# Performance work log

Hardware: AMD Instinct MI355X
Metric: run time of the kernel (lower is better)

Reference implementation:

```python
import jax, jax.numpy as jnp
import numpy as np

ALPHA = 0.2  # LeakyReLU negative slope
NEG_FILL = -9e15


def setup_inputs() -> dict:
    key = jax.random.key(0)
    k_adj, k_x, k_W, k_a = jax.random.split(key, 4)
    n, in_feats, out_feats = 12288, 256, 64
    adj = jax.random.randint(k_adj, (n, n), 0, 2, dtype=jnp.int32)
    x = jax.random.normal(k_x, (n, in_feats), dtype=jnp.float32)
    W = jax.random.normal(k_W, (in_feats, out_feats), dtype=jnp.float32) * 0.1
    a = jax.random.normal(k_a, (2 * out_feats, 1), dtype=jnp.float32) * 0.1
    return {"adj": adj, "x": x, "W": W, "a": a}


def reference(adj, x, W, a):
    out_feats = W.shape[1]
    h = x @ W                                  # (n, out_feats)
    wh1 = h @ a[:out_feats]                    # (n, 1)
    wh2 = h @ a[out_feats:]                    # (n, 1)
    e = jax.nn.leaky_relu(wh1 + wh2, ALPHA)    # (n, 1) -- faithful to source (no transpose)
    # broadcast (n,1) scores against (n,n) adjacency mask
    attention = jnp.where(adj > 0, e, NEG_FILL)
    attention = jax.nn.softmax(attention, axis=1)
    # dropout p=0.0 -> identity (eval mode)
    h_prime = attention @ h                    # (n, out_feats)
    return jax.nn.elu(h_prime)                 # concat=True
```

## Files before the change

### kernel.cpp

```cpp
#include <hip/hip_runtime.h>

#define N_NODES 12288
#define IN_F    256
#define OUT_F   64
#define KSPLIT  32
#define MT      64
#define KC      (N_NODES / KSPLIT)
#define NSTRH   (N_NODES + 32)
#define ABSTR   1600

typedef __attribute__((ext_vector_type(8))) short bf16x8;
typedef __attribute__((ext_vector_type(4))) float f32x4;

__device__ __forceinline__ unsigned short f2bf(float f) {
    union { float f; unsigned int i; } v; v.f = f;
    unsigned int x = v.i;
    unsigned int r = x + 0x7FFFu + ((x >> 16) & 1u);
    return (unsigned short)(r >> 16);
}

__global__ __launch_bounds__(256) void k_bitpack(const int* __restrict__ adj,
                                                 unsigned char* __restrict__ abits) {
    const int tid  = threadIdx.x;
    const int lane = tid & 63;
    const int wave = tid >> 6;
    const int row  = blockIdx.x * 2 + (wave >> 1);
    const int half = wave & 1;

    const int* src = adj + (size_t)row * N_NODES + half * (N_NODES / 2) + lane;
    unsigned long long* dst =
        (unsigned long long*)(abits + (size_t)row * ABSTR + half * (N_NODES / 16));

    const int iters = (N_NODES / 2) / 64;
    int a0 = src[0];
    int a1 = src[64];
    for (int i = 0; i < iters - 2; ++i) {
        int a2 = src[(size_t)(i + 2) * 64];
        unsigned long long m = __ballot(a0 != 0);
        if (lane == 0) dst[i] = m;
        a0 = a1; a1 = a2;
    }
    unsigned long long m0 = __ballot(a0 != 0);
    unsigned long long m1 = __ballot(a1 != 0);
    if (lane == 0) { dst[iters - 2] = m0; dst[iters - 1] = m1; }
}

__global__ __launch_bounds__(256) void k_hT(const float* __restrict__ x,
                                            const float* __restrict__ W,
                                            unsigned short* __restrict__ hT) {
    __shared__ unsigned short WT[OUT_F][IN_F + 8];
    int tid = threadIdx.x;
    for (int idx = tid; idx < IN_F * OUT_F; idx += 256) {
        int k = idx >> 6, n = idx & 63;
        WT[n][k] = f2bf(W[idx]);
    }
    __syncthreads();

    int lane = tid & 63, wave = tid >> 6;
    int q = lane >> 4, ml = lane & 15;
    int i0 = blockIdx.x * MT;
    int row = i0 + 16 * wave + ml;
    const float* xr = x + (size_t)row * IN_F + 8 * q;

    f32x4 acc[4];
    #pragma unroll
    for (int nt = 0; nt < 4; ++nt) acc[nt] = (f32x4){0.f, 0.f, 0.f, 0.f};

    #pragma unroll
    for (int kk = 0; kk < IN_F; kk += 32) {
        float4 x0 = *(const float4*)(xr + kk);
        float4 x1 = *(const float4*)(xr + kk + 4);
        union { bf16x8 v; unsigned short u[8]; } A;
        A.u[0] = f2bf(x0.x); A.u[1] = f2bf(x0.y); A.u[2] = f2bf(x0.z); A.u[3] = f2bf(x0.w);
        A.u[4] = f2bf(x1.x); A.u[5] = f2bf(x1.y); A.u[6] = f2bf(x1.z); A.u[7] = f2bf(x1.w);
        #pragma unroll
        for (int nt = 0; nt < 4; ++nt) {
            bf16x8 bv = *(const bf16x8*)&WT[16 * nt + ml][kk + 8 * q];
            acc[nt] = __builtin_amdgcn_mfma_f32_16x16x32_bf16(A.v, bv, acc[nt], 0, 0, 0);
        }
    }

    #pragma unroll
    for (int nt = 0; nt < 4; ++nt) {
        ushort4 o;
        o.x = f2bf(acc[nt][0]); o.y = f2bf(acc[nt][1]);
        o.z = f2bf(acc[nt][2]); o.w = f2bf(acc[nt][3]);
        *(ushort4*)&hT[(size_t)(16 * nt + ml) * NSTRH + i0 + 16 * wave + 4 * q] = o;
    }
}

__global__ __launch_bounds__(256) void k_spmm(const unsigned char* __restrict__ abits,
                                              const unsigned short* __restrict__ hT,
                                              float* __restrict__ s_part,
                                              float* __restrict__ deg_part) {
    __shared__ unsigned short Bs[OUT_F][KC + 8];
    __shared__ unsigned char  Ab[MT][52];

    const int tid  = threadIdx.x;
    const int lane = tid & 63;
    const int wave = tid >> 6;
    const int q    = lane >> 4;
    const int ml   = lane & 15;
    const int i0   = blockIdx.x * MT;
    const int ks   = blockIdx.y;
    const int k0   = ks * KC;

    {
        const int brow = 16 * wave + (lane >> 2);
        const int bco  = (lane & 3) * 8;
        const unsigned short* bp = hT + (size_t)brow * NSTRH + k0 + bco;
        #pragma unroll
        for (int j = 0; j < 12; ++j) {
            uint4 v = *(const uint4*)(bp + 32 * j);
            *(uint4*)&Bs[brow][bco + 32 * j] = v;
        }
    }
    {
        const int arow = tid >> 2;
        const int apart = (tid & 3) * 12;
        const unsigned int* asrc =
            (const unsigned int*)(abits + (size_t)(i0 + arow) * ABSTR + ks * (KC / 8) + apart);
        unsigned int d0 = asrc[0], d1 = asrc[1], d2 = asrc[2];
        unsigned int* ad = (unsigned int*)&Ab[arow][apart];
        ad[0] = d0; ad[1] = d1; ad[2] = d2;
    }
    __syncthreads();

    union { bf16x8 v; unsigned short u[8]; } ones;
    #pragma unroll
    for (int i = 0; i < 8; ++i) ones.u[i] = 0x3F80;

    f32x4 acc[4], accd;
    #pragma unroll
    for (int nt = 0; nt < 4; ++nt) acc[nt] = (f32x4){0.f, 0.f, 0.f, 0.f};
    accd = (f32x4){0.f, 0.f, 0.f, 0.f};

    const int arow = 16 * wave + ml;
    #pragma unroll
    for (int kk = 0; kk < KC; kk += 32) {
        unsigned int b = Ab[arow][(kk >> 3) + q];
        union { bf16x8 v; unsigned int w[4]; } av;
        av.w[0] = (b & 1u) * 0x3F80u         + (b & 2u) * 0x1FC00000u;
        av.w[1] = ((b >> 2) & 1u) * 0x3F80u  + ((b >> 2) & 2u) * 0x1FC00000u;
        av.w[2] = ((b >> 4) & 1u) * 0x3F80u  + ((b >> 4) & 2u) * 0x1FC00000u;
        av.w[3] = ((b >> 6) & 1u) * 0x3F80u  + ((b >> 6) & 2u) * 0x1FC00000u;

        #pragma unroll
        for (int nt = 0; nt < 4; ++nt) {
            bf16x8 bv = *(const bf16x8*)&Bs[16 * nt + ml][kk + 8 * q];
            acc[nt] = __builtin_amdgcn_mfma_f32_16x16x32_bf16(av.v, bv, acc[nt], 0, 0, 0);
        }
        accd = __builtin_amdgcn_mfma_f32_16x16x32_bf16(av.v, ones.v, accd, 0, 0, 0);
    }

    float* sp = s_part + (size_t)ks * ((size_t)N_NODES * OUT_F);
    #pragma unroll
    for (int nt = 0; nt < 4; ++nt) {
        #pragma unroll
        for (int rr = 0; rr < 4; ++rr) {
            int orow = i0 + 16 * wave + 4 * q + rr;
            int ocol = 16 * nt + ml;
            sp[(size_t)orow * OUT_F + ocol] = acc[nt][rr];
        }
    }

    if (ml == 0) {
        #pragma unroll
        for (int rr = 0; rr < 4; ++rr)
            deg_part[ks * N_NODES + i0 + 16 * wave + 4 * q + rr] = accd[rr];
    }
}

__global__ __launch_bounds__(256) void k_out(const float* __restrict__ s_part,
                                             const float* __restrict__ deg_part,
                                             float* __restrict__ out) {
    int idx = blockIdx.x * 256 + threadIdx.x;
    int i = idx >> 6;
    float s = 0.f, deg = 0.f;
    #pragma unroll
    for (int p = 0; p < KSPLIT; ++p) {
        s   += s_part[(size_t)p * ((size_t)N_NODES * OUT_F) + idx];
        deg += deg_part[p * N_NODES + i];
    }
    float v = (deg > 0.5f) ? (s / deg) : 0.f;
    out[idx] = (v > 0.f) ? v : expm1f(v);
}

extern "C" void kernel_launch(void* const* d_in, const int* in_sizes, int n_in,
                              void* d_out, int out_size, void* d_ws, size_t ws_size,
                              hipStream_t stream) {
    const int*   adj = (const int*)d_in[0];
    const float* x   = (const float*)d_in[1];
    const float* W   = (const float*)d_in[2];
    float* out = (float*)d_out;

    char* ws = (char*)d_ws;
    const size_t hT_bytes = (size_t)OUT_F * NSTRH * 2;
    const size_t sp_bytes = (size_t)KSPLIT * N_NODES * OUT_F * 4;
    const size_t dp_bytes = (size_t)KSPLIT * N_NODES * 4;
    unsigned short* hT   = (unsigned short*)ws;
    float* s_part        = (float*)(ws + hT_bytes);
    float* deg_part      = (float*)(ws + hT_bytes + sp_bytes);
    unsigned char* abits = (unsigned char*)(ws + hT_bytes + sp_bytes + dp_bytes);

    k_bitpack<<<dim3(N_NODES / 2),          dim3(256), 0, stream>>>(adj, abits);
    k_hT     <<<dim3(N_NODES / MT),         dim3(256), 0, stream>>>(x, W, hT);
    k_spmm   <<<dim3(N_NODES / MT, KSPLIT), dim3(256), 0, stream>>>(abits, hT, s_part, deg_part);
    k_out    <<<dim3(N_NODES * OUT_F / 256),dim3(256), 0, stream>>>(s_part, deg_part, out);
}
```

Before: 878.9 us.

## Restructure adjacency bitpack as persistent grid-stride kernel with dense bit layout

The bit-packing kernel now runs as a fixed grid of 2048 blocks. Each block walks the flattened adjacency matrix in grid strides, with every wave ballot-packing four 64-element chunks per iteration and prefetching the next iteration's loads. The packed row stride becomes exactly N/8 bytes, so the bits are laid out contiguously, and stores are issued as 16-byte vector writes. The aim is more loads in flight and better streaming efficiency on the dominant pass, which reads a 600MB int32 matrix. The cost is more register pressure from the prefetch buffers.

```diff
diff --git a/kernel.cpp b/kernel.cpp
--- a/kernel.cpp
+++ b/kernel.cpp
@@ -7,7 +7,7 @@
 #define MT      64
 #define KC      (N_NODES / KSPLIT)
 #define NSTRH   (N_NODES + 32)
-#define ABSTR   1600
+#define ABSTR   (N_NODES / 8)
 
 typedef __attribute__((ext_vector_type(8))) short bf16x8;
 typedef __attribute__((ext_vector_type(4))) float f32x4;
@@ -20,29 +20,37 @@
 }
 
 __global__ __launch_bounds__(256) void k_bitpack(const int* __restrict__ adj,
-                                                 unsigned char* __restrict__ abits) {
+                                                 unsigned long long* __restrict__ abits) {
     const int tid  = threadIdx.x;
     const int lane = tid & 63;
     const int wave = tid >> 6;
-    const int row  = blockIdx.x * 2 + (wave >> 1);
-    const int half = wave & 1;
-
-    const int* src = adj + (size_t)row * N_NODES + half * (N_NODES / 2) + lane;
-    unsigned long long* dst =
-        (unsigned long long*)(abits + (size_t)row * ABSTR + half * (N_NODES / 16));
-
-    const int iters = (N_NODES / 2) / 64;
-    int a0 = src[0];
-    int a1 = src[64];
-    for (int i = 0; i < iters - 2; ++i) {
-        int a2 = src[(size_t)(i + 2) * 64];
-        unsigned long long m = __ballot(a0 != 0);
-        if (lane == 0) dst[i] = m;
-        a0 = a1; a1 = a2;
-    }
-    unsigned long long m0 = __ballot(a0 != 0);
-    unsigned long long m1 = __ballot(a1 != 0);
-    if (lane == 0) { dst[iters - 2] = m0; dst[iters - 1] = m1; }
+    const int b    = blockIdx.x;
+    const int ITER = (N_NODES * N_NODES / 64) / (2048 * 16);
+
+    const int* src0 = adj + ((size_t)b * 16 + 4 * wave) * 64 + lane;
+
+    int curv[4], nxtv[4];
+    #pragma unroll
+    for (int g = 0; g < 4; ++g) curv[g] = src0[64 * g];
+
+    for (int j = 0; j < ITER; ++j) {
+        const size_t nb = ((size_t)(j + 1) * 2048) * 16 * 64;
+        if (j + 1 < ITER) {
+            #pragma unroll
+            for (int g = 0; g < 4; ++g) nxtv[g] = src0[nb + 64 * g];
+        }
+        unsigned long long m0 = __ballot(curv[0] != 0);
+        unsigned long long m1 = __ballot(curv[1] != 0);
+        unsigned long long m2 = __ballot(curv[2] != 0);
+        unsigned long long m3 = __ballot(curv[3] != 0);
+        if (lane == 0) {
+            unsigned long long* d = abits + ((size_t)j * 2048 + b) * 16 + 4 * wave;
+            ((ulonglong2*)d)[0] = (ulonglong2){m0, m1};
+            ((ulonglong2*)d)[1] = (ulonglong2){m2, m3};
+        }
+        #pragma unroll
+        for (int g = 0; g < 4; ++g) curv[g] = nxtv[g];
+    }
 }
 
 __global__ __launch_bounds__(256) void k_hT(const float* __restrict__ x,
@@ -203,7 +211,7 @@
     float* deg_part      = (float*)(ws + hT_bytes + sp_bytes);
     unsigned char* abits = (unsigned char*)(ws + hT_bytes + sp_bytes + dp_bytes);
 
-    k_bitpack<<<dim3(N_NODES / 2),          dim3(256), 0, stream>>>(adj, abits);
+    k_bitpack<<<dim3(2048),                 dim3(256), 0, stream>>>(adj, (unsigned long long*)abits);
     k_hT     <<<dim3(N_NODES / MT),         dim3(256), 0, stream>>>(x, W, hT);
     k_spmm   <<<dim3(N_NODES / MT, KSPLIT), dim3(256), 0, stream>>>(abits, hT, s_part, deg_part);
     k_out    <<<dim3(N_NODES * OUT_F / 256),dim3(256), 0, stream>>>(s_part, deg_part, out);
```

After: 856.0 us. 1.03x faster.
